# Performance work log

Hardware: AMD Instinct MI355X
Metric: run time of the kernel (lower is better)

## Reference

```python
import jax, jax.numpy as jnp
import numpy as np

ITEM_NUM = 50000
TARGET_ITEM_NUM = 50000
EMB = 128
N_LAYERS = 3
N_EDGES = 800000
N_NODES = ITEM_NUM + 1  # forward uses item_emb[:item_num+1]


def gcn_conv(x, row, col, W, b, n):
    """PyG GCNConv: symmetric-normalized aggregation with self-loops.
    out = D^{-1/2} (A + I) D^{-1/2} (x @ W) + b
    """
    h = x @ W  # [n, d]
    loops = jnp.arange(n)
    r = jnp.concatenate([row, loops])  # source
    c = jnp.concatenate([col, loops])  # target
    deg = jax.ops.segment_sum(jnp.ones(r.shape[0], x.dtype), c, num_segments=n)
    dinv = jnp.where(deg > 0, deg ** -0.5, jnp.zeros_like(deg))
    norm = dinv[r] * dinv[c]  # [E+n]
    out = jax.ops.segment_sum(h[r] * norm[:, None], c, num_segments=n)
    return out + b


def setup_inputs() -> dict:
    key = jax.random.key(0)
    k0, k1, k2 = jax.random.split(key, 3)
    edge_index = jax.random.randint(k0, (2, N_EDGES), 0, N_NODES)
    total = ITEM_NUM + TARGET_ITEM_NUM + 1
    # xavier_uniform for embedding table and per-layer GCN weights
    lim_e = float(np.sqrt(6.0 / (total + EMB)))
    item_emb = jax.random.uniform(k1, (total, EMB), jnp.float32, -lim_e, lim_e)
    lim_w = float(np.sqrt(6.0 / (EMB + EMB)))
    W = jax.random.uniform(k2, (N_LAYERS, EMB, EMB), jnp.float32, -lim_w, lim_w)
    b = jnp.zeros((N_LAYERS, EMB), jnp.float32)
    return {"edge_index": edge_index, "item_emb": item_emb, "W": W, "b": b}


def reference(edge_index, item_emb, W, b):
    n = N_NODES
    row, col = edge_index[0], edge_index[1]
    embeds = [item_emb[:n]]
    for i in range(N_LAYERS):
        embeds.append(gcn_conv(embeds[-1], row, col, W[i], b[i], n))
    return sum(embeds)  # [n, EMB], sum over layer embeddings
```

## Files before the change

### kernel.cpp

```cpp
#include <hip/hip_runtime.h>
#include <hip/hip_bf16.h>


constexpr int NN   = 50001;
constexpr int D    = 128;
constexpr int NPAD = 50048;
constexpr int NBK  = 196;
constexpr int CAP  = 7680;
constexpr int ZROW = NPAD - 1;

using bf16x8 = __attribute__((ext_vector_type(8))) short;
using f32x4  = __attribute__((ext_vector_type(4))) float;
using f32x2  = __attribute__((ext_vector_type(2))) float;
using u16x8  = __attribute__((ext_vector_type(8))) unsigned short;
using u32x4  = __attribute__((ext_vector_type(4))) unsigned;

__device__ __forceinline__ ushort f2b(float f) {
    unsigned u = __float_as_uint(f);
    return (ushort)((u + 0x7FFFu + ((u >> 16) & 1u)) >> 16);
}
__device__ __forceinline__ float b2f(ushort u) {
    return __uint_as_float((unsigned)u << 16);
}

__global__ __launch_bounds__(256)
void k_build(const int* __restrict__ row, const int* __restrict__ col,
             int* __restrict__ partCur, unsigned* __restrict__ part,
             const float* __restrict__ W, ushort* __restrict__ Wt,
             const float* __restrict__ emb, ushort* __restrict__ xb, int E, int n) {
    int b = blockIdx.x, t = threadIdx.x;
    if (b < NBK) {
        __shared__ int hist[256];
        __shared__ int base[256];
        hist[t] = 0;
        __syncthreads();
        int e0 = b * 4096;
        unsigned rec[16];
        int bkt[16];
#pragma unroll
        for (int k = 0; k < 16; k++) {
            int e = e0 + k * 256 + t;
            if (e < E) {
                int r = row[e], c = col[e];
                rec[k] = (unsigned)r | ((unsigned)(c & 255) << 16);
                bkt[k] = c >> 8;
                atomicAdd(&hist[bkt[k]], 1);
            } else bkt[k] = -1;
        }
        __syncthreads();
        if (hist[t] > 0) base[t] = t * CAP + atomicAdd(&partCur[t], hist[t]);
        __syncthreads();
#pragma unroll
        for (int k = 0; k < 16; k++) {
            if (bkt[k] >= 0) {
                int pos = atomicAdd(&base[bkt[k]], 1);
                if (pos < (bkt[k] + 1) * CAP) part[pos] = rec[k];
            }
        }
    } else if (b < NBK + 192) {
        int idx = (b - NBK) * 256 + t;
        int l = idx >> 14, rem = idx & 16383;
        int c = rem >> 7, k = rem & 127;
        Wt[idx] = f2b(W[l * D * D + k * D + c]);
    } else {
        int i4 = (b - NBK - 192) * 256 + t;
        if (i4 >= NPAD * (D / 4)) return;
        int r = i4 >> 5;
        if (r < n) {
            float4 v = ((const float4*)emb)[i4];
            ushort4 o; o.x = f2b(v.x); o.y = f2b(v.y); o.z = f2b(v.z); o.w = f2b(v.w);
            ((ushort4*)xb)[i4] = o;
        } else {
            ((ushort4*)xb)[i4] = make_ushort4(0, 0, 0, 0);
        }
    }
}

__global__ __launch_bounds__(256)
void k_scat(const unsigned* __restrict__ part, const int* __restrict__ partCur,
            float* __restrict__ dinv, unsigned* __restrict__ rp,
            ushort* __restrict__ meta, int n) {
    __shared__ int hist[256];
    __shared__ int sm[256];
    __shared__ int off[256];
    __shared__ int cur[256];
    int b = blockIdx.x, t = threadIdx.x;
    int node0 = b * 256;
    int nn = min(256, n - node0);
    int T = min(partCur[b], CAP);
    const unsigned* pb = part + (size_t)b * CAP;
    hist[t] = 0;
    __syncthreads();
    for (int i = t; i < T; i += 256) atomicAdd(&hist[pb[i] >> 16], 1);
    __syncthreads();
    int v = hist[t];
    int pv = (v + 15) & ~15;
    sm[t] = pv;
    __syncthreads();
    for (int ofs = 1; ofs < 256; ofs <<= 1) {
        int u = (t >= ofs) ? sm[t - ofs] : 0;
        __syncthreads();
        sm[t] += u;
        __syncthreads();
    }
    off[t] = sm[t] - pv;
    cur[t] = 0;
    if (t < nn) {
        dinv[node0 + t] = rsqrtf((float)v + 1.0f);
        rp[node0 + t] = (unsigned)(b * CAP + off[t]) | ((unsigned)v << 21);
    }
    __syncthreads();
    for (int i = t; i < T; i += 256) {
        unsigned rec = pb[i];
        int dl = (int)(rec >> 16);
        int pos = off[dl] + atomicAdd(&cur[dl], 1);
        if (pos < CAP) meta[(size_t)b * CAP + pos] = (ushort)(rec & 0xFFFFu);
    }
    int base = off[t];
    for (int p = v; p < pv; p++)
        if (base + p < CAP) meta[(size_t)b * CAP + base + p] = (ushort)ZROW;
}

constexpr int WT_LD = 136;
__global__ __launch_bounds__(256)
void k_gemm_mfma(const ushort* __restrict__ xb, const ushort* __restrict__ WtL,
                 const float* __restrict__ dinv, ushort* __restrict__ h, int n) {
    __shared__ ushort wlds[D * WT_LD];
    for (int idx = threadIdx.x; idx < D * (D / 8); idx += 256) {
        int r = idx >> 4, c8 = (idx & 15) * 8;
        *(uint4*)&wlds[r * WT_LD + c8] = *(const uint4*)&WtL[r * D + c8];
    }
    __syncthreads();

    int wave = threadIdx.x >> 6, lane = threadIdx.x & 63;
    int q = lane >> 4, i = lane & 15;
    int waveRow = blockIdx.x * 128 + wave * 32;

    bf16x8 a[2][4];
#pragma unroll
    for (int rt = 0; rt < 2; rt++) {
        const ushort* base = &xb[(size_t)(waveRow + rt * 16 + i) * D + q * 8];
#pragma unroll
        for (int ks = 0; ks < 4; ks++)
            a[rt][ks] = *(const bf16x8*)(base + ks * 32);
    }

    f32x4 acc[2][8] = {};
#pragma unroll
    for (int ct = 0; ct < 8; ct++) {
        const ushort* wbase = &wlds[(ct * 16 + i) * WT_LD + q * 8];
#pragma unroll
        for (int ks = 0; ks < 4; ks++) {
            bf16x8 bfr = *(const bf16x8*)(wbase + ks * 32);
            acc[0][ct] = __builtin_amdgcn_mfma_f32_16x16x32_bf16(a[0][ks], bfr, acc[0][ct], 0, 0, 0);
            acc[1][ct] = __builtin_amdgcn_mfma_f32_16x16x32_bf16(a[1][ks], bfr, acc[1][ct], 0, 0, 0);
        }
    }

#pragma unroll
    for (int rt = 0; rt < 2; rt++)
#pragma unroll
        for (int r4 = 0; r4 < 4; r4++) {
            int row = waveRow + rt * 16 + q * 4 + r4;
            float dv = (row < n) ? dinv[row] : 0.f;
#pragma unroll
            for (int ct = 0; ct < 8; ct++)
                h[(size_t)row * D + ct * 16 + i] = f2b(acc[rt][ct][r4] * dv);
        }
}

__global__ __launch_bounds__(256)
void k_pull(const unsigned* __restrict__ rp, const ushort* __restrict__ meta,
            const ushort* __restrict__ h,
            const float* __restrict__ dinv, const float* __restrict__ bias,
            ushort* __restrict__ xb_out,
            const float* __restrict__ emb, const ushort* __restrict__ x1,
            const ushort* __restrict__ x2, float* __restrict__ out,
            int n, int mode) {
    int node = blockIdx.x * 16 + (threadIdx.x >> 4);
    int l    = threadIdx.x & 15;
    if (node >= n) {
        if (mode == 0) {
            u16x8 z = {0, 0, 0, 0, 0, 0, 0, 0};
            *(u16x8*)(xb_out + (size_t)node * D + (l << 3)) = z;
        }
        return;
    }
    unsigned pk = rp[node];
    int s   = (int)(pk & 0x1FFFFFu);
    int deg = (int)(pk >> 21);
    size_t o = (size_t)node * D + (l << 3);

    const ushort* hl = h + (l << 3);

    u32x4 sv = *(const u32x4*)(hl + (size_t)node * D);
    float di = dinv[node];
    const float4* bp = (const float4*)(bias + (l << 3));
    float4 b0 = bp[0], b1 = bp[1];
    float4 e0, e1; u16x8 w1, w2;
    if (mode) {
        const float4* ep = (const float4*)(emb + o);
        e0 = ep[0]; e1 = ep[1];
        w1 = *(const u16x8*)(x1 + o);
        w2 = *(const u16x8*)(x2 + o);
    }

    float accL[4], accH[4];
#pragma unroll
    for (int k = 0; k < 4; k++) {
        accL[k] = __uint_as_float(sv[k] << 16);
        accH[k] = __uint_as_float(sv[k] & 0xFFFF0000u);
    }

    for (int j = 0; j < deg; j += 16) {
        u16x8 m0 = *(const u16x8*)&meta[s + j];
        u16x8 m1 = *(const u16x8*)&meta[s + j + 8];
        u32x4 v[16];
#pragma unroll
        for (int u = 0; u < 8; u++) v[u]     = *(const u32x4*)(hl + (size_t)m0[u] * D);
#pragma unroll
        for (int u = 0; u < 8; u++) v[8 + u] = *(const u32x4*)(hl + (size_t)m1[u] * D);
#pragma unroll
        for (int u = 0; u < 16; u++)
#pragma unroll
            for (int k = 0; k < 4; k++) {
                accL[k] += __uint_as_float(v[u][k] << 16);
                accH[k] += __uint_as_float(v[u][k] & 0xFFFF0000u);
            }
    }

    float r0 = fmaf(accL[0], di, b0.x);
    float r1 = fmaf(accH[0], di, b0.y);
    float r2 = fmaf(accL[1], di, b0.z);
    float r3 = fmaf(accH[1], di, b0.w);
    float r4 = fmaf(accL[2], di, b1.x);
    float r5 = fmaf(accH[2], di, b1.y);
    float r6 = fmaf(accL[3], di, b1.z);
    float r7 = fmaf(accH[3], di, b1.w);
    if (mode == 0) {
        u16x8 w;
        w[0] = f2b(r0); w[1] = f2b(r1); w[2] = f2b(r2); w[3] = f2b(r3);
        w[4] = f2b(r4); w[5] = f2b(r5); w[6] = f2b(r6); w[7] = f2b(r7);
        *(u16x8*)(xb_out + o) = w;
    } else {
        f32x4 o0, o1;
        o0[0] = e0.x + b2f(w1[0]) + b2f(w2[0]) + r0;
        o0[1] = e0.y + b2f(w1[1]) + b2f(w2[1]) + r1;
        o0[2] = e0.z + b2f(w1[2]) + b2f(w2[2]) + r2;
        o0[3] = e0.w + b2f(w1[3]) + b2f(w2[3]) + r3;
        o1[0] = e1.x + b2f(w1[4]) + b2f(w2[4]) + r4;
        o1[1] = e1.y + b2f(w1[5]) + b2f(w2[5]) + r5;
        o1[2] = e1.z + b2f(w1[6]) + b2f(w2[6]) + r6;
        o1[3] = e1.w + b2f(w1[7]) + b2f(w2[7]) + r7;
        __builtin_nontemporal_store(o0, (f32x4*)(out + o));
        __builtin_nontemporal_store(o1, (f32x4*)(out + o) + 1);
    }
}

extern "C" void kernel_launch(void* const* d_in, const int* in_sizes, int n_in,
                              void* d_out, int out_size, void* d_ws, size_t ws_size,
                              hipStream_t stream) {
    const int*   edge = (const int*)d_in[0];
    const float* emb  = (const float*)d_in[1];
    const float* W    = (const float*)d_in[2];
    const float* b    = (const float*)d_in[3];
    float* out = (float*)d_out;

    const int E = in_sizes[0] / 2;
    const int n = NN;
    const int* row = edge;
    const int* col = edge + E;

    char* ws = (char*)d_ws;
    size_t off = 0;
    auto carve = [&](size_t bytes) { char* p = ws + off; off = (off + bytes + 511) / 512 * 512; return p; };
    int*      partCur = (int*)     carve(256 * 4);
    unsigned* part    = (unsigned*)carve((size_t)NBK * CAP * 4);
    ushort*   meta    = (ushort*)  carve((size_t)NBK * CAP * 2);
    unsigned* rp      = (unsigned*)carve((size_t)n * 4);
    float*    dinv    = (float*)   carve((size_t)n * 4);
    ushort*   Wt      = (ushort*)  carve((size_t)3 * D * D * 2);
    ushort*   xb0     = (ushort*)  carve((size_t)NPAD * D * 2);
    ushort*   xb1     = (ushort*)  carve((size_t)NPAD * D * 2);
    ushort*   xb2     = (ushort*)  carve((size_t)NPAD * D * 2);
    ushort*   h       = (ushort*)  carve((size_t)NPAD * D * 2);

    (void)hipMemsetAsync(partCur, 0, 256 * 4, stream);

    const int init_blocks  = (NPAD * (D / 4) + 255) / 256;
    const int build_blocks = NBK + 192 + init_blocks;
    k_build<<<build_blocks, 256, 0, stream>>>(row, col, partCur, part, W, Wt, emb, xb0, E, n);
    k_scat <<<NBK, 256, 0, stream>>>(part, partCur, dinv, rp, meta, n);

    const int gemm_blocks = NPAD / 128;
    const int pull_blocks = NPAD / 16;
    ushort* xin[3]  = {xb0, xb1, xb2};
    ushort* xout[3] = {xb1, xb2, nullptr};
    for (int l = 0; l < 3; l++) {
        k_gemm_mfma<<<gemm_blocks, 256, 0, stream>>>(xin[l], Wt + (size_t)l * D * D, dinv, h, n);
        k_pull<<<pull_blocks, 256, 0, stream>>>(rp, meta, h,
                                                dinv, b + (size_t)l * D, xout[l],
                                                emb, xb1, xb2, out, n, (l < 2) ? 0 : 1);
    }
}
```

Measured before the change: 248.7 us.

## Fuse next-layer GEMM into aggregation kernel, ping-pong h buffers

```diff
diff --git a/kernel.cpp b/kernel.cpp
--- a/kernel.cpp
+++ b/kernel.cpp
@@ -11,7 +11,6 @@
 
 using bf16x8 = __attribute__((ext_vector_type(8))) short;
 using f32x4  = __attribute__((ext_vector_type(4))) float;
-using f32x2  = __attribute__((ext_vector_type(2))) float;
 using u16x8  = __attribute__((ext_vector_type(8))) unsigned short;
 using u32x4  = __attribute__((ext_vector_type(4))) unsigned;
 
@@ -170,40 +169,121 @@
 }
 
 __global__ __launch_bounds__(256)
-void k_pull(const unsigned* __restrict__ rp, const ushort* __restrict__ meta,
-            const ushort* __restrict__ h,
-            const float* __restrict__ dinv, const float* __restrict__ bias,
-            ushort* __restrict__ xb_out,
-            const float* __restrict__ emb, const ushort* __restrict__ x1,
-            const ushort* __restrict__ x2, float* __restrict__ out,
-            int n, int mode) {
+void k_fused(const unsigned* __restrict__ rp, const ushort* __restrict__ meta,
+             const ushort* __restrict__ h_in,
+             const float* __restrict__ dinv, const float* __restrict__ bias,
+             const ushort* __restrict__ Wn,
+             ushort* __restrict__ xb_out, ushort* __restrict__ h_out, int n) {
+    __shared__ ushort xlds[16 * WT_LD];
+    __shared__ float  sdinv[16];
+    int tid  = threadIdx.x;
+    int nl   = tid >> 4;
+    int l    = tid & 15;
+    int node0 = blockIdx.x * 16;
+    int node  = node0 + nl;
+
+    u16x8 w = {0, 0, 0, 0, 0, 0, 0, 0};
+    float di = 0.f;
+    if (node < n) {
+        unsigned pk = rp[node];
+        int s   = (int)(pk & 0x1FFFFFu);
+        int deg = (int)(pk >> 21);
+        const ushort* hl = h_in + (l << 3);
+
+        u32x4 sv = *(const u32x4*)(hl + (size_t)node * D);
+        di = dinv[node];
+        const float4* bp = (const float4*)(bias + (l << 3));
+        float4 b0 = bp[0], b1 = bp[1];
+
+        float accL[4], accH[4];
+#pragma unroll
+        for (int k = 0; k < 4; k++) {
+            accL[k] = __uint_as_float(sv[k] << 16);
+            accH[k] = __uint_as_float(sv[k] & 0xFFFF0000u);
+        }
+        for (int j = 0; j < deg; j += 16) {
+            u16x8 m0 = *(const u16x8*)&meta[s + j];
+            u16x8 m1 = *(const u16x8*)&meta[s + j + 8];
+            u32x4 v[16];
+#pragma unroll
+            for (int u = 0; u < 8; u++) v[u]     = *(const u32x4*)(hl + (size_t)m0[u] * D);
+#pragma unroll
+            for (int u = 0; u < 8; u++) v[8 + u] = *(const u32x4*)(hl + (size_t)m1[u] * D);
+#pragma unroll
+            for (int u = 0; u < 16; u++)
+#pragma unroll
+                for (int k = 0; k < 4; k++) {
+                    accL[k] += __uint_as_float(v[u][k] << 16);
+                    accH[k] += __uint_as_float(v[u][k] & 0xFFFF0000u);
+                }
+        }
+        w[0] = f2b(fmaf(accL[0], di, b0.x));
+        w[1] = f2b(fmaf(accH[0], di, b0.y));
+        w[2] = f2b(fmaf(accL[1], di, b0.z));
+        w[3] = f2b(fmaf(accH[1], di, b0.w));
+        w[4] = f2b(fmaf(accL[2], di, b1.x));
+        w[5] = f2b(fmaf(accH[2], di, b1.y));
+        w[6] = f2b(fmaf(accL[3], di, b1.z));
+        w[7] = f2b(fmaf(accH[3], di, b1.w));
+        *(u16x8*)(xb_out + (size_t)node * D + (l << 3)) = w;
+    }
+    *(u16x8*)&xlds[nl * WT_LD + l * 8] = w;
+    if (l == 0) sdinv[nl] = di;
+    __syncthreads();
+
+    int wave = tid >> 6, lane = tid & 63;
+    int q = lane >> 4, i = lane & 15;
+
+    bf16x8 a[4];
+#pragma unroll
+    for (int ks = 0; ks < 4; ks++)
+        a[ks] = *(const bf16x8*)&xlds[i * WT_LD + ks * 32 + q * 8];
+
+    f32x4 acc[2] = {};
+#pragma unroll
+    for (int ct = 0; ct < 2; ct++) {
+        const ushort* wbase = &Wn[(size_t)(wave * 32 + ct * 16 + i) * D + q * 8];
+#pragma unroll
+        for (int ks = 0; ks < 4; ks++) {
+            bf16x8 bfr = *(const bf16x8*)(wbase + ks * 32);
+            acc[ct] = __builtin_amdgcn_mfma_f32_16x16x32_bf16(a[ks], bfr, acc[ct], 0, 0, 0);
+        }
+    }
+
+#pragma unroll
+    for (int r4 = 0; r4 < 4; r4++) {
+        int rr = q * 4 + r4;
+        float dv = sdinv[rr];
+#pragma unroll
+        for (int ct = 0; ct < 2; ct++)
+            h_out[(size_t)(node0 + rr) * D + wave * 32 + ct * 16 + i] =
+                f2b(acc[ct][r4] * dv);
+    }
+}
+
+__global__ __launch_bounds__(256)
+void k_pull_final(const unsigned* __restrict__ rp, const ushort* __restrict__ meta,
+                  const ushort* __restrict__ h,
+                  const float* __restrict__ dinv, const float* __restrict__ bias,
+                  const float* __restrict__ emb, const ushort* __restrict__ x1,
+                  const ushort* __restrict__ x2, float* __restrict__ out, int n) {
     int node = blockIdx.x * 16 + (threadIdx.x >> 4);
     int l    = threadIdx.x & 15;
-    if (node >= n) {
-        if (mode == 0) {
-            u16x8 z = {0, 0, 0, 0, 0, 0, 0, 0};
-            *(u16x8*)(xb_out + (size_t)node * D + (l << 3)) = z;
-        }
-        return;
-    }
+    if (node >= n) return;
     unsigned pk = rp[node];
     int s   = (int)(pk & 0x1FFFFFu);
     int deg = (int)(pk >> 21);
     size_t o = (size_t)node * D + (l << 3);
-
     const ushort* hl = h + (l << 3);
 
     u32x4 sv = *(const u32x4*)(hl + (size_t)node * D);
     float di = dinv[node];
     const float4* bp = (const float4*)(bias + (l << 3));
     float4 b0 = bp[0], b1 = bp[1];
-    float4 e0, e1; u16x8 w1, w2;
-    if (mode) {
-        const float4* ep = (const float4*)(emb + o);
-        e0 = ep[0]; e1 = ep[1];
-        w1 = *(const u16x8*)(x1 + o);
-        w2 = *(const u16x8*)(x2 + o);
-    }
+    const float4* ep = (const float4*)(emb + o);
+    float4 e0 = ep[0], e1 = ep[1];
+    u16x8 w1 = *(const u16x8*)(x1 + o);
+    u16x8 w2 = *(const u16x8*)(x2 + o);
 
     float accL[4], accH[4];
 #pragma unroll
@@ -211,7 +291,6 @@
         accL[k] = __uint_as_float(sv[k] << 16);
         accH[k] = __uint_as_float(sv[k] & 0xFFFF0000u);
     }
-
     for (int j = 0; j < deg; j += 16) {
         u16x8 m0 = *(const u16x8*)&meta[s + j];
         u16x8 m1 = *(const u16x8*)&meta[s + j + 8];
@@ -228,33 +307,17 @@
                 accH[k] += __uint_as_float(v[u][k] & 0xFFFF0000u);
             }
     }
-
-    float r0 = fmaf(accL[0], di, b0.x);
-    float r1 = fmaf(accH[0], di, b0.y);
-    float r2 = fmaf(accL[1], di, b0.z);
-    float r3 = fmaf(accH[1], di, b0.w);
-    float r4 = fmaf(accL[2], di, b1.x);
-    float r5 = fmaf(accH[2], di, b1.y);
-    float r6 = fmaf(accL[3], di, b1.z);
-    float r7 = fmaf(accH[3], di, b1.w);
-    if (mode == 0) {
-        u16x8 w;
-        w[0] = f2b(r0); w[1] = f2b(r1); w[2] = f2b(r2); w[3] = f2b(r3);
-        w[4] = f2b(r4); w[5] = f2b(r5); w[6] = f2b(r6); w[7] = f2b(r7);
-        *(u16x8*)(xb_out + o) = w;
-    } else {
-        f32x4 o0, o1;
-        o0[0] = e0.x + b2f(w1[0]) + b2f(w2[0]) + r0;
-        o0[1] = e0.y + b2f(w1[1]) + b2f(w2[1]) + r1;
-        o0[2] = e0.z + b2f(w1[2]) + b2f(w2[2]) + r2;
-        o0[3] = e0.w + b2f(w1[3]) + b2f(w2[3]) + r3;
-        o1[0] = e1.x + b2f(w1[4]) + b2f(w2[4]) + r4;
-        o1[1] = e1.y + b2f(w1[5]) + b2f(w2[5]) + r5;
-        o1[2] = e1.z + b2f(w1[6]) + b2f(w2[6]) + r6;
-        o1[3] = e1.w + b2f(w1[7]) + b2f(w2[7]) + r7;
-        __builtin_nontemporal_store(o0, (f32x4*)(out + o));
-        __builtin_nontemporal_store(o1, (f32x4*)(out + o) + 1);
-    }
+    f32x4 o0, o1;
+    o0[0] = e0.x + b2f(w1[0]) + b2f(w2[0]) + fmaf(accL[0], di, b0.x);
+    o0[1] = e0.y + b2f(w1[1]) + b2f(w2[1]) + fmaf(accH[0], di, b0.y);
+    o0[2] = e0.z + b2f(w1[2]) + b2f(w2[2]) + fmaf(accL[1], di, b0.z);
+    o0[3] = e0.w + b2f(w1[3]) + b2f(w2[3]) + fmaf(accH[1], di, b0.w);
+    o1[0] = e1.x + b2f(w1[4]) + b2f(w2[4]) + fmaf(accL[2], di, b1.x);
+    o1[1] = e1.y + b2f(w1[5]) + b2f(w2[5]) + fmaf(accH[2], di, b1.y);
+    o1[2] = e1.z + b2f(w1[6]) + b2f(w2[6]) + fmaf(accL[3], di, b1.z);
+    o1[3] = e1.w + b2f(w1[7]) + b2f(w2[7]) + fmaf(accH[3], di, b1.w);
+    __builtin_nontemporal_store(o0, (f32x4*)(out + o));
+    __builtin_nontemporal_store(o1, (f32x4*)(out + o) + 1);
 }
 
 extern "C" void kernel_launch(void* const* d_in, const int* in_sizes, int n_in,
@@ -283,7 +346,8 @@
     ushort*   xb0     = (ushort*)  carve((size_t)NPAD * D * 2);
     ushort*   xb1     = (ushort*)  carve((size_t)NPAD * D * 2);
     ushort*   xb2     = (ushort*)  carve((size_t)NPAD * D * 2);
-    ushort*   h       = (ushort*)  carve((size_t)NPAD * D * 2);
+    ushort*   hA      = (ushort*)  carve((size_t)NPAD * D * 2);
+    ushort*   hB      = (ushort*)  carve((size_t)NPAD * D * 2);
 
     (void)hipMemsetAsync(partCur, 0, 256 * 4, stream);
 
@@ -292,14 +356,15 @@
     k_build<<<build_blocks, 256, 0, stream>>>(row, col, partCur, part, W, Wt, emb, xb0, E, n);
     k_scat <<<NBK, 256, 0, stream>>>(part, partCur, dinv, rp, meta, n);
 
-    const int gemm_blocks = NPAD / 128;
-    const int pull_blocks = NPAD / 16;
-    ushort* xin[3]  = {xb0, xb1, xb2};
-    ushort* xout[3] = {xb1, xb2, nullptr};
-    for (int l = 0; l < 3; l++) {
-        k_gemm_mfma<<<gemm_blocks, 256, 0, stream>>>(xin[l], Wt + (size_t)l * D * D, dinv, h, n);
-        k_pull<<<pull_blocks, 256, 0, stream>>>(rp, meta, h,
-                                                dinv, b + (size_t)l * D, xout[l],
-                                                emb, xb1, xb2, out, n, (l < 2) ? 0 : 1);
-    }
-}
+    const int gemm_blocks  = NPAD / 128;
+    const int fused_blocks = NPAD / 16;
+    const int final_blocks = (n + 15) / 16;
+
+    k_gemm_mfma<<<gemm_blocks, 256, 0, stream>>>(xb0, Wt, dinv, hA, n);
+    k_fused<<<fused_blocks, 256, 0, stream>>>(rp, meta, hA, dinv, b,
+                                              Wt + (size_t)1 * D * D, xb1, hB, n);
+    k_fused<<<fused_blocks, 256, 0, stream>>>(rp, meta, hB, dinv, b + D,
+                                              Wt + (size_t)2 * D * D, xb2, hA, n);
+    k_pull_final<<<final_blocks, 256, 0, stream>>>(rp, meta, hA, dinv, b + 2 * D,
+                                                   emb, xb1, xb2, out, n);
+}
```

New measurement: 240.5 us (median of 2 runs). 3.3% less time.
